# Kernel optimization log

Hardware: AMD Instinct MI355X
Metric: run time of the kernel (lower is better)

## Reference

```python
import jax, jax.numpy as jnp
import numpy as np

B, NT, DIM, HEADS = 8, 16, 768, 8
RES_H = RES_W = 32
PIX = RES_H * RES_W              # 1024
CHAN_NH = 16
NH = NW = 4                      # sqrt(chan_nheads)
WH, WW = RES_H // NH, RES_W // NW  # 8, 8
HEAD_DIM = DIM // HEADS          # 96
CHAN_HEAD_DIM = PIX // CHAN_NH   # 64


def _linear(x, w, b=None):
    y = x @ w.T
    return y if b is None else y + b


def _quat_kernel(r, i, j, k):
    # Hamilton-product block kernel: (4*out_c, 4*in_c, K)
    row_r = jnp.concatenate([r, -i, -j, -k], axis=1)
    row_i = jnp.concatenate([i, r, -k, j], axis=1)
    row_j = jnp.concatenate([j, k, r, -i], axis=1)
    row_k = jnp.concatenate([k, -j, i, r], axis=1)
    return jnp.concatenate([row_r, row_i, row_j, row_k], axis=0)


def _conv1d(x, w, b=None, pad=1):
    y = jax.lax.conv_general_dilated(x, w, (1,), [(pad, pad)],
                                     dimension_numbers=('NCH', 'OIH', 'NCH'))
    return y if b is None else y + b[None, :, None]


def _win(z, t):
    # 'b t (nh h nw w) -> b (nh nw) t (h w)'
    b = z.shape[0]
    z = z.reshape(b, t, NH, WH, NW, WW).transpose(0, 2, 4, 1, 3, 5)
    return z.reshape(b, NH * NW, t, WH * WW)


def setup_inputs():
    key = jax.random.key(0)
    ks = jax.random.split(key, 24)
    s = lambda i, shape: jax.random.normal(ks[i], shape, dtype=jnp.float32) * 0.02
    return dict(
        x=jax.random.normal(ks[0], (B, PIX, DIM), jnp.float32),
        task_prompts=jax.random.normal(ks[1], (B, NT, DIM), jnp.float32),
        qkv_w=s(2, (3 * DIM, DIM)),
        proj_w=s(3, (DIM, DIM)), proj_b=s(4, (DIM,)),
        tt_w=s(5, (PIX, DIM)), tt_b=s(6, (PIX,)),
        tt1_w=s(7, (DIM, PIX)), tt1_b=s(8, (DIM,)),
        qf_r=s(9, (2, 1, 3)), qf_i=s(10, (2, 1, 3)), qf_j=s(11, (2, 1, 3)),
        qf_k=s(12, (2, 1, 3)), qf_b=s(13, (8,)),
        dqf_r=s(14, (2, 1, 3)), dqf_i=s(15, (2, 1, 3)), dqf_j=s(16, (2, 1, 3)),
        dqf_k=s(17, (2, 1, 3)), dqf_b=s(18, (4,)),
        bn_g=jnp.ones((4,), jnp.float32), bn_b=jnp.zeros((4,), jnp.float32),
        qfto_w=s(19, (1, 4, 1)),
    )


def reference(x, task_prompts, qkv_w, proj_w, proj_b, tt_w, tt_b, tt1_w, tt1_b,
              qf_r, qf_i, qf_j, qf_k, qf_b, dqf_r, dqf_i, dqf_j, dqf_k, dqf_b,
              bn_g, bn_b, qfto_w):
    # ---- spatial attention over [prompts ; pixels] ----
    xc = jnp.concatenate([task_prompts, x], axis=1)           # (B, N, C), N = NT + PIX
    b, n, c = xc.shape
    qkv = _linear(xc, qkv_w).reshape(b, n, 3, HEADS, HEAD_DIM).transpose(2, 0, 3, 1, 4)
    q, k, v = qkv[0], qkv[1], qkv[2]
    raw_spa = jnp.einsum('bhqd,bhkd->bhqk', q, k)             # pre-scale logits (returned)
    spa_attn = jax.nn.softmax(raw_spa * HEAD_DIM ** -0.5, axis=-1)
    out = jnp.einsum('bhqk,bhkd->bhqd', spa_attn, v).transpose(0, 2, 1, 3).reshape(b, n, c)
    out = _linear(out, proj_w, proj_b)
    tp_out, x_out = out[:, :-PIX, :], out[:, -PIX:, :]        # sep_prompt(x, -pixel_no)

    # ---- windowed channel attention ----
    chan_x = x[:, -PIX:, :]                                   # (B, PIX, C)
    chan_prompts = _linear(task_prompts, tt_w, tt_b)          # (B, NT, PIX)
    qw = _win(chan_prompts, NT)                               # (B, 16, NT, 64)
    kw = _win(chan_x.transpose(0, 2, 1), DIM)                 # (B, 16, C, 64)
    raw_chan = jnp.einsum('bwtd,bwcd->bwtc', qw, kw)          # (B, 16, NT, C)
    chan_attn = jax.nn.softmax(raw_chan * CHAN_HEAD_DIM ** -0.5, axis=-1)
    # chan_x output of attn@v is computed in torch but unused downstream; XLA DCEs it.
    raw_chan_r = raw_chan.reshape(b, NH, NW, NT, DIM).transpose(0, 3, 4, 1, 2)   # b t c nh nw
    chan_attn_r = chan_attn.reshape(b, NH, NW, NT, DIM).transpose(0, 3, 4, 1, 2)

    # ---- quaternion fusion of prompt streams (vectorized over the torch per-sample loop) ----
    ch_prompts = _linear(chan_prompts, tt1_w, tt1_b)          # (B, NT, C)
    zero = jnp.zeros_like(tp_out)
    quater = jnp.stack([zero, task_prompts, tp_out, ch_prompts], axis=2)  # (B, NT, 4, C)
    w1 = _quat_kernel(qf_r, qf_i, qf_j, qf_k)                 # (8, 4, 3), OIH
    fe = _conv1d(quater.reshape(b * NT, 4, DIM), w1, qf_b)    # (B*NT, 8, C)
    w2 = _quat_kernel(dqf_r, dqf_i, dqf_j, dqf_k)             # (8, 4, 3) as (in, out, K)
    w2c = jnp.flip(w2, -1).transpose(1, 0, 2)                 # conv_transpose1d(s=1,p=1) == conv1d(flip, p=K-1-1)
    fe = _conv1d(fe, w2c, dqf_b).reshape(b, NT, 4, DIM)       # (B, NT, 4, C)
    # BatchNorm1d(4) in training mode, stats per loop iteration => per-sample over (NT, C)
    mean = fe.mean(axis=(1, 3), keepdims=True)
    var = fe.var(axis=(1, 3), keepdims=True)
    fe = (fe - mean) / jnp.sqrt(var + 1e-5) * bn_g[None, None, :, None] + bn_b[None, None, :, None]
    fe = jax.nn.gelu(fe, approximate=False)
    quater_out = jnp.einsum('bnkc,k->bnc', fe, qfto_w[0, :, 0])  # Conv1d(4,1,k=1,no bias)
    return (x_out, raw_spa, spa_attn, raw_chan_r, chan_attn_r, quater_out)
```

## Files before the change

kernel.cpp:

```cpp
#include <hip/hip_runtime.h>
#include <hip/hip_bf16.h>
#include <math.h>

typedef unsigned short u16;
typedef __attribute__((ext_vector_type(8))) short  bf16x8;
typedef __attribute__((ext_vector_type(4))) float  f32x4;
typedef __attribute__((ext_vector_type(8))) u16    u16x8;
typedef __attribute__((ext_vector_type(4))) u16    u16x4;

#define B_      8
#define NT_     16
#define DIM_    768
#define HEADS_  8
#define HD_     96
#define PIX_    1024
#define NTOK_   1040
#define NPAD_   1152

#define WSO_XCB     0ull
#define WSO_WQKV    12779520ull
#define WSO_WPROJ   16318464ull
#define WSO_QB      17498112ull
#define WSO_KB      31653888ull
#define WSO_VB      45809664ull
// ... 58 lines not shown
    if (bx < 3120) {
        size_t idx8 = ((size_t)bx * 256 + tid) * 8;
        int c = idx8 % DIM_;
        int n = (idx8 / DIM_) % NTOK_;
        int b = idx8 / ((size_t)DIM_ * NTOK_);
        s = (n < NT_) ? tp + ((size_t)b * NT_ + n) * DIM_ + c
                      : x + ((size_t)b * PIX_ + (n - NT_)) * DIM_ + c;
        d8 = xcb + idx8;
    } else {
        int i = (bx - 3120) * 256 + tid;
        const float* src;
        u16* dst;
        int li;
        if (i < 221184)      { src = qkv_w;  dst = wqkvb;  li = i; }
        else if (i < 294912) { src = proj_w; dst = wprojb; li = i - 221184; }
        else if (i < 307200) { src = tp;     dst = tpb;    li = i - 294912; }
        else if (i < 405504) { src = tt_w;   dst = ttwb;   li = i - 307200; }
        else if (i < 503808) { src = tt1_w;  dst = tt1wb;  li = i - 405504; }
        else return;
        s = src + (size_t)li * 8;
        d8 = dst + (size_t)li * 8;
    }
    float4 a = *(const float4*)s;
    float4 d = *(const float4*)(s + 4);
    u16x8 r;
    r[0] = f2b(a.x); r[1] = f2b(a.y); r[2] = f2b(a.z); r[3] = f2b(a.w);
    r[4] = f2b(d.x); r[5] = f2b(d.y); r[6] = f2b(d.z); r[7] = f2b(d.w);
    *(u16x8*)d8 = r;
}

template <int MODE>
__global__ __launch_bounds__(256) void gemm_bf16(
    const u16* __restrict__ A, const u16* __restrict__ Bw,
    int lda, int ldb, int K, size_t strA, size_t strB,
    const float* __restrict__ bias,
    float* __restrict__ o0, float* __restrict__ o1,
    u16* __restrict__ oq, u16* __restrict__ ok, u16* __restrict__ ov,
    int ldo) {
    __shared__ u16 As[128 * 32];
    __shared__ u16 Bs[128 * 32];
    __shared__ float redm[128][2];
    __shared__ float reds[128][2];
    const int tid = threadIdx.x;
    const int bm = blockIdx.x, bn = blockIdx.y, z = blockIdx.z;
    const u16* Ab = A + strA * z;
    const u16* Bb = Bw + strB * z;
    const int lane = tid & 63, wid = tid >> 6;
    const int ln = lane & 15, hi = lane >> 4;
    const int wr = wid >> 1, wc = wid & 1;
    const int lrow = lane >> 2;
    const int lcol = (lane & 3) * 8;
    f32x4 acc[4][4] = {};
    for (int kt = 0; kt < K; kt += 32) {
        __syncthreads();
#pragma unroll
        for (int t = 0; t < 2; ++t) {
            int rowbase = t * 64 + wid * 16;
            const u16* ga = Ab + (size_t)(bm * 128 + rowbase + lrow) * lda + kt + lcol;
            const u16* gb = Bb + (size_t)(bn * 128 + rowbase + lrow) * ldb + kt + lcol;
            gload_lds16(ga, &As[rowbase * 32]);
            gload_lds16(gb, &Bs[rowbase * 32]);
        }
        __syncthreads();
        bf16x8 af[4], bfr[4];
#pragma unroll
        for (int m = 0; m < 4; ++m)
            af[m] = *(const bf16x8*)&As[(wr * 64 + m * 16 + ln) * 32 + hi * 8];
#pragma unroll
        for (int n = 0; n < 4; ++n)
            bfr[n] = *(const bf16x8*)&Bs[(wc * 64 + n * 16 + ln) * 32 + hi * 8];
#pragma unroll
        for (int m = 0; m < 4; ++m)
#pragma unroll
            for (int n = 0; n < 4; ++n)
                acc[m][n] = __builtin_amdgcn_mfma_f32_16x16x32_bf16(af[m], bfr[n], acc[m][n], 0, 0, 0);
    }
#pragma unroll
    for (int m = 0; m < 4; ++m) {
#pragma unroll
        for (int n = 0; n < 4; ++n) {
#pragma unroll
            for (int j = 0; j < 4; ++j) {
                int gm = bm * 128 + wr * 64 + m * 16 + hi * 4 + j;
                int gn = bn * 128 + wc * 64 + n * 16 + ln;
                float v = acc[m][n][j];
                if (MODE == 0) {
                    int b = gm / NTOK_, nn = gm - b * NTOK_;
                    int s = gn / DIM_, rem = gn - s * DIM_;
                    int h = rem / HD_, d = rem - h * HD_;
                    u16 hv = f2b(v);
                    u16* dst = (s == 0) ? oq : (s == 1) ? ok : ov;
                    dst[(((size_t)b * HEADS_ + h) * NPAD_ + nn) * HD_ + d] = hv;
                } else if (MODE == 1) {
                    if (gm < NTOK_ && gn < NTOK_)
                        __builtin_nontemporal_store(v, &o0[((size_t)z * NTOK_ + gm) * NTOK_ + gn]);
                } else if (MODE == 2) {
                    v += bias[gn];
                    int b = gm / NTOK_, nn = gm - b * NTOK_;
                    if (nn < NT_) o1[((size_t)b * NT_ + nn) * DIM_ + gn] = v;
                    else          __builtin_nontemporal_store(v, &o0[((size_t)b * PIX_ + (nn - NT_)) * DIM_ + gn]);
                } else if (MODE == 3) {
                    oq[(size_t)gm * ldo + gn] = f2b(v + bias[gn]);
                } else {
                    o0[(size_t)gm * ldo + gn] = v + bias[gn];
                }
            }
        }
    }
    if (MODE == 1) {
#pragma unroll
        for (int m = 0; m < 4; ++m) {
#pragma unroll
            for (int j = 0; j < 4; ++j) {
                float v[4];
                float mx = -INFINITY;
#pragma unroll
                for (int n = 0; n < 4; ++n) {
                    int gn = bn * 128 + wc * 64 + n * 16 + ln;
                    v[n] = (gn < NTOK_) ? acc[m][n][j] * SCALE_SPA : -INFINITY;
                    mx = fmaxf(mx, v[n]);
                }
#pragma unroll
                for (int off = 1; off < 16; off <<= 1) mx = fmaxf(mx, __shfl_xor(mx, off));
                float s = 0.f;
                if (mx > -INFINITY) {
#pragma unroll
                    for (int n = 0; n < 4; ++n)
                        if (v[n] > -INFINITY) s += __expf(v[n] - mx);
                }
#pragma unroll
                for (int off = 1; off < 16; off <<= 1) s += __shfl_xor(s, off);
                if (ln == 0) {
                    int row = wr * 64 + m * 16 + hi * 4 + j;
                    redm[row][wc] = mx;
                    reds[row][wc] = s;
                }
            }
        }
        __syncthreads();
        if (tid < 128) {
            float m0 = redm[tid][0], m1 = redm[tid][1];
            float s0 = reds[tid][0], s1 = reds[tid][1];
            float M = fmaxf(m0, m1);
            float S = 0.f;
            if (m0 > -INFINITY) S += s0 * __expf(m0 - M);
            if (m1 > -INFINITY) S += s1 * __expf(m1 - M);
            float2* pp = (float2*)o1;
            pp[((size_t)z * 9 + bn) * NPAD_ + bm * 128 + tid] = make_float2(M, S);
        }
    }
}

__global__ __launch_bounds__(256) void transpose_v(const u16* __restrict__ vb,
                                                   u16* __restrict__ vtb) {
    __shared__ u16 t[32][34];
    int bi = blockIdx.x, bj = blockIdx.y, z = blockIdx.z;
    const u16* ib = vb + (size_t)z * NPAD_ * HD_;
    u16* ob = vtb + (size_t)z * HD_ * NPAD_;
    int tid = threadIdx.x;
    int r = tid >> 3, c = (tid & 7) * 4;
    *(u16x4*)&t[r][c] = *(const u16x4*)(ib + (size_t)(bi * 32 + r) * HD_ + bj * 32 + c);
    __syncthreads();
    u16x4 o;
    o[0] = t[c + 0][r]; o[1] = t[c + 1][r]; o[2] = t[c + 2][r]; o[3] = t[c + 3][r];
    *(u16x4*)(ob + (size_t)(bj * 32 + r) * NPAD_ + bi * 32 + c) = o;
}

__global__ __launch_bounds__(256) void attn_pv4(const float* __restrict__ raw,
                                                const float2* __restrict__ part,
                                                const u16* __restrict__ vtb,
                                                float* __restrict__ attn,
                                                u16* __restrict__ acat) {
    __shared__ u16 Ps[64][136];
    __shared__ float sm[64], si[64];
    const int tid = threadIdx.x;
    const int bi = blockIdx.x, z = blockIdx.y;
    const int lane = tid & 63, wid = tid >> 6;
    const int ln = lane & 15, hi = lane >> 4;
    const int wr = wid >> 1, wc = wid & 1;
    const int r0 = tid >> 3, c8 = tid & 7;
    const u16* vbz = vtb + (size_t)z * HD_ * NPAD_;
    const float* rawz = raw + (size_t)z * NTOK_ * NTOK_;
    float* attnz = attn + (size_t)z * NTOK_ * NTOK_;
    int rows[2];
    bool vr[2];
#pragma unroll
    for (int p = 0; p < 2; ++p) {
        rows[p] = bi * 64 + p * 32 + r0;
        vr[p] = rows[p] < NTOK_;
    }
    f32x4 rcur[4][2], rnxt[4][2];
#pragma unroll
    for (int s = 0; s < 4; ++s) {
        int col = s * 32 + c8 * 4;
#pragma unroll
        for (int p = 0; p < 2; ++p) {
            f32x4 zv = {0.f, 0.f, 0.f, 0.f};
            if (vr[p] && col < NTOK_)
                zv = __builtin_nontemporal_load((const f32x4*)(rawz + (size_t)rows[p] * NTOK_ + col));
            rcur[s][p] = zv;
        }
    }
    if (tid < 64) {
        int grow = bi * 64 + tid;
        float M = -INFINITY;
        float mj[9], sj[9];
#pragma unroll
        for (int jt = 0; jt < 9; ++jt) {
            float2 p = part[((size_t)z * 9 + jt) * NPAD_ + grow];
            mj[jt] = p.x; sj[jt] = p.y;
            M = fmaxf(M, p.x);
        }
        float S = 0.f;
#pragma unroll
        for (int jt = 0; jt < 9; ++jt)
            if (mj[jt] > -INFINITY) S += sj[jt] * __expf(mj[jt] - M);
        sm[tid] = M;
        si[tid] = 1.f / S;
    }
    __syncthreads();
    float mr[2], ir[2];
#pragma unroll
    for (int p = 0; p < 2; ++p) {
        mr[p] = sm[p * 32 + r0];
        ir[p] = si[p * 32 + r0];
    }
    f32x4 oacc[2][3] = {};
    for (int ci = 0; ci < 9; ++ci) {
        const int c0 = ci * 128;
#pragma unroll
        for (int s = 0; s < 4; ++s) {
            int cl = s * 32 + c8 * 4;
            int col = c0 + cl;
#pragma unroll
            for (int p = 0; p < 2; ++p) {
                int rr = p * 32 + r0;
                u16x4 pb = {0, 0, 0, 0};
                if (vr[p] && col < NTOK_) {
                    f32x4 v = rcur[s][p];
                    f32x4 pr;
                    pr[0] = __expf(v[0] * SCALE_SPA - mr[p]) * ir[p];
                    pr[1] = __expf(v[1] * SCALE_SPA - mr[p]) * ir[p];
                    pr[2] = __expf(v[2] * SCALE_SPA - mr[p]) * ir[p];
                    pr[3] = __expf(v[3] * SCALE_SPA - mr[p]) * ir[p];
                    __builtin_nontemporal_store(pr, (f32x4*)(attnz + (size_t)rows[p] * NTOK_ + col));
                    pb[0] = f2b_fast(pr[0]); pb[1] = f2b_fast(pr[1]);
                    pb[2] = f2b_fast(pr[2]); pb[3] = f2b_fast(pr[3]);
                }
                *(u16x4*)&Ps[rr][cl] = pb;
            }
        }
        if (ci < 8) {
#pragma unroll
            for (int s = 0; s < 4; ++s) {
                int col = c0 + 128 + s * 32 + c8 * 4;
#pragma unroll
                for (int p = 0; p < 2; ++p) {
                    f32x4 zv = {0.f, 0.f, 0.f, 0.f};
                    if (vr[p] && col < NTOK_)
                        zv = __builtin_nontemporal_load((const f32x4*)(rawz + (size_t)rows[p] * NTOK_ + col));
                    rnxt[s][p] = zv;
                }
            }
        }
        __syncthreads();
#pragma unroll
        for (int ktl = 0; ktl < 4; ++ktl) {
            bf16x8 af[2];
#pragma unroll
            for (int m = 0; m < 2; ++m)
                af[m] = *(const bf16x8*)&Ps[wr * 32 + m * 16 + ln][ktl * 32 + hi * 8];
#pragma unroll
            for (int n = 0; n < 3; ++n) {
                bf16x8 bv = *(const bf16x8*)(vbz + (size_t)(wc * 48 + n * 16 + ln) * NPAD_
                                             + c0 + ktl * 32 + hi * 8);
#pragma unroll
                for (int m = 0; m < 2; ++m)
                    oacc[m][n] = __builtin_amdgcn_mfma_f32_16x16x32_bf16(af[m], bv, oacc[m][n], 0, 0, 0);
            }
        }
        __syncthreads();
#pragma unroll
        for (int s = 0; s < 4; ++s)
#pragma unroll
            for (int p = 0; p < 2; ++p)
                rcur[s][p] = rnxt[s][p];
    }
    const int b = z >> 3, h = z & 7;
#pragma unroll
    for (int m = 0; m < 2; ++m)
#pragma unroll
        for (int n = 0; n < 3; ++n)
#pragma unroll
            for (int j = 0; j < 4; ++j) {
                int gi = bi * 64 + wr * 32 + m * 16 + hi * 4 + j;
                if (gi < NTOK_) {
                    int gd = wc * 48 + n * 16 + ln;
                    acat[((size_t)b * NTOK_ + gi) * DIM_ + h * HD_ + gd] = f2b(oacc[m][n][j]);
                }
            }
}

__global__ __launch_bounds__(256) void chan_scores(const u16* __restrict__ chanpb,
                                                   const float* __restrict__ x,
                                                   float* __restrict__ rawchan_ws,
                                                   float* __restrict__ out_raw) {
    int blk = blockIdx.x;
    int b = blk / 16, w = blk % 16;
    int cy = blockIdx.y;
    int nh = w / 4, nw = w % 4;
    __shared__ float qp[16][65];
    __shared__ float xs[64][17];
    int tid = threadIdx.x;
    for (int l = tid; l < 16 * 64; l += 256) {
        int t = l / 64, d = l % 64;
        int wh = d / 8, ww = d % 8;
        int pix = (nh * 8 + wh) * 32 + nw * 8 + ww;
        qp[t][d] = b2f(chanpb[((size_t)b * NT_ + t) * PIX_ + pix]);
    }
    __syncthreads();
    int t = tid % 16, cl = tid / 16;
    for (int cc = cy * 8; cc < cy * 8 + 8; ++cc) {
        for (int l = tid; l < 64 * 16; l += 256) {
            int d = l / 16, c2 = l % 16;
            int wh = d / 8, ww = d % 8;
            int pix = (nh * 8 + wh) * 32 + nw * 8 + ww;
            xs[d][c2] = x[((size_t)b * PIX_ + pix) * DIM_ + cc * 16 + c2];
        }
        __syncthreads();
        float acc = 0.f;
#pragma unroll
        for (int d = 0; d < 64; ++d) acc += qp[t][d] * xs[d][cl];
        int c = cc * 16 + cl;
        rawchan_ws[(((size_t)b * 16 + w) * NT_ + t) * DIM_ + c] = acc;
        out_raw[(((size_t)b * NT_ + t) * DIM_ + c) * 16 + w] = acc;
        __syncthreads();
    }
}

__global__ __launch_bounds__(256) void chan_softmax(const float* __restrict__ rawchan_ws,
                                                    float* __restrict__ out_attn) {
    int row = blockIdx.x;
    int b = row / 256;
    int w = (row / 16) % 16;
    int t = row % 16;
    const float* rp = rawchan_ws + (size_t)row * DIM_;
    int tid = threadIdx.x;
    float vals[3];
    float m = -INFINITY;
#pragma unroll
    for (int i = 0; i < 3; ++i) {
        vals[i] = rp[tid + i * 256] * 0.125f;
        m = fmaxf(m, vals[i]);
    }
    __shared__ float redm[4], reds[4];
    for (int off = 32; off; off >>= 1) m = fmaxf(m, __shfl_xor(m, off));
    if ((tid & 63) == 0) redm[tid >> 6] = m;
    __syncthreads();
    m = fmaxf(fmaxf(redm[0], redm[1]), fmaxf(redm[2], redm[3]));
    float s = 0.f;
#pragma unroll
    for (int i = 0; i < 3; ++i) { vals[i] = __expf(vals[i] - m); s += vals[i]; }
    for (int off = 32; off; off >>= 1) s += __shfl_xor(s, off);
    if ((tid & 63) == 0) reds[tid >> 6] = s;
    __syncthreads();
    s = reds[0] + reds[1] + reds[2] + reds[3];
    float inv = 1.f / s;
#pragma unroll
    for (int i = 0; i < 3; ++i) {
        int c = tid + i * 256;
        out_attn[(((size_t)b * NT_ + t) * DIM_ + c) * 16 + w] = vals[i] * inv;
    }
}

__global__ __launch_bounds__(256) void quat_conv(const float* __restrict__ tp,
                                                 const float* __restrict__ tpo,
                                                 const float* __restrict__ chp,
                                                 const float* __restrict__ qf_r, const float* __restrict__ qf_i,
                                                 const float* __restrict__ qf_j, const float* __restrict__ qf_k,
                                                 const float* __restrict__ qf_b,
                                                 const float* __restrict__ dqf_r, const float* __restrict__ dqf_i,
                                                 const float* __restrict__ dqf_j, const float* __restrict__ dqf_k,
                                                 const float* __restrict__ dqf_b,
                                                 float* __restrict__ fe2_out,
                                                 float* __restrict__ partials) {
    int blk = blockIdx.x;
    int b = blk / NT_, t = blk % NT_;
    __shared__ float w1[8][4][3];
    __shared__ float w2[8][4][3];
    __shared__ float w2c[4][8][3];
    __shared__ float qs[4][770];
    __shared__ float fs[8][770];
    __shared__ float wsum[4][4], wsq[4][4];
    int tid = threadIdx.x;
    if (tid < 96) {
        int o = tid / 12, rest = tid % 12, ic = rest / 3, tap = rest % 3;
        int g = o / 2, oo = o % 2;
        const int   cidx[4][4] = {{0, 1, 2, 3}, {1, 0, 3, 2}, {2, 3, 0, 1}, {3, 2, 1, 0}};
        const float csgn[4][4] = {{1, -1, -1, -1}, {1, 1, -1, 1}, {1, 1, 1, -1}, {1, -1, 1, 1}};
        const float* s1[4] = {qf_r, qf_i, qf_j, qf_k};
        const float* s2[4] = {dqf_r, dqf_i, dqf_j, dqf_k};
        w1[o][ic][tap] = csgn[g][ic] * s1[cidx[g][ic]][oo * 3 + tap];
        w2[o][ic][tap] = csgn[g][ic] * s2[cidx[g][ic]][oo * 3 + tap];
    }
    for (int l = tid; l < DIM_; l += 256) {
        size_t base = ((size_t)b * NT_ + t) * DIM_ + l;
        qs[0][1 + l] = 0.f;
        qs[1][1 + l] = tp[base];
        qs[2][1 + l] = tpo[base];
        qs[3][1 + l] = chp[base];
    }
    if (tid < 4) { qs[tid][0] = 0.f; qs[tid][769] = 0.f; }
    if (tid < 8) { fs[tid][0] = 0.f; fs[tid][769] = 0.f; }
    __syncthreads();
    if (tid < 96) {
        int o2 = tid / 24, rest = tid % 24, i2 = rest / 3, tap = rest % 3;
        w2c[o2][i2][tap] = w2[i2][o2][2 - tap];
    }
    for (int l = tid; l < DIM_; l += 256) {
#pragma unroll
        for (int o = 0; o < 8; ++o) {
            float a = qf_b[o];
#pragma unroll
            for (int ic = 0; ic < 4; ++ic)
#pragma unroll
                for (int tap = 0; tap < 3; ++tap) a += w1[o][ic][tap] * qs[ic][l + tap];
            fs[o][1 + l] = a;
        }
    }
    __syncthreads();
    float lsum[4] = {}, lsq[4] = {};
    for (int l = tid; l < DIM_; l += 256) {
#pragma unroll
        for (int o2 = 0; o2 < 4; ++o2) {
            float a = dqf_b[o2];
#pragma unroll
            for (int i2 = 0; i2 < 8; ++i2)
#pragma unroll
                for (int tap = 0; tap < 3; ++tap) a += w2c[o2][i2][tap] * fs[i2][l + tap];
            fe2_out[((size_t)blk * 4 + o2) * DIM_ + l] = a;
            lsum[o2] += a;
            lsq[o2] += a * a;
        }
    }
    int wid = tid >> 6;
#pragma unroll
    for (int o2 = 0; o2 < 4; ++o2) {
        float s = lsum[o2], q = lsq[o2];
        for (int off = 32; off; off >>= 1) { s += __shfl_xor(s, off); q += __shfl_xor(q, off); }
        if ((tid & 63) == 0) { wsum[wid][o2] = s; wsq[wid][o2] = q; }
    }
    __syncthreads();
    if (tid < 4) {
        float s = wsum[0][tid] + wsum[1][tid] + wsum[2][tid] + wsum[3][tid];
        float q = wsq[0][tid] + wsq[1][tid] + wsq[2][tid] + wsq[3][tid];
        partials[(size_t)blk * 8 + tid * 2 + 0] = s;
        partials[(size_t)blk * 8 + tid * 2 + 1] = q;
    }
}

__global__ __launch_bounds__(256) void bn_gelu_out(const float* __restrict__ fe2,
                                                   const float* __restrict__ partials,
                                                   const float* __restrict__ bn_g,
                                                   const float* __restrict__ bn_b,
                                                   const float* __restrict__ qfto,
                                                   float* __restrict__ out5) {
    int blk = blockIdx.x;
    int b = blk / NT_;
    int tid = threadIdx.x;
    float mean[4], rstd[4], gam[4], bet[4], qw[4];
#pragma unroll
    for (int kk = 0; kk < 4; ++kk) {
        float s = 0.f, q = 0.f;
        for (int t2 = 0; t2 < 16; ++t2) {
            const float* p = partials + ((size_t)(b * NT_ + t2) * 8 + kk * 2);
            s += p[0];
            q += p[1];
        }
        float mu = s * (1.f / 12288.f);
        float var = q * (1.f / 12288.f) - mu * mu;
        mean[kk] = mu;
        rstd[kk] = rsqrtf(var + 1e-5f);
        gam[kk] = bn_g[kk];
        bet[kk] = bn_b[kk];
        qw[kk] = qfto[kk];
    }
    for (int l = tid; l < DIM_; l += 256) {
        float acc = 0.f;
#pragma unroll
        for (int kk = 0; kk < 4; ++kk) {
// ... 26 lines not shown
    const float* dqf_r  = (const float*)d_in[14];
    const float* dqf_i  = (const float*)d_in[15];
    const float* dqf_j  = (const float*)d_in[16];
    const float* dqf_k  = (const float*)d_in[17];
    const float* dqf_b  = (const float*)d_in[18];
    const float* bn_g   = (const float*)d_in[19];
    const float* bn_b   = (const float*)d_in[20];
    const float* qfto   = (const float*)d_in[21];
    float* out = (float*)d_out;
    char* wsb = (char*)d_ws;

    u16* xcb    = (u16*)(wsb + WSO_XCB);
    u16* wqkvb  = (u16*)(wsb + WSO_WQKV);
    u16* wprojb = (u16*)(wsb + WSO_WPROJ);
    u16* qb     = (u16*)(wsb + WSO_QB);
    u16* kb     = (u16*)(wsb + WSO_KB);
    u16* vb     = (u16*)(wsb + WSO_VB);
    u16* vtb    = (u16*)(wsb + WSO_VTB);
    u16* acatb  = (u16*)(wsb + WSO_ACATB);
    u16* tpb    = (u16*)(wsb + WSO_TPB);
    u16* ttwb   = (u16*)(wsb + WSO_TTWB);
    u16* tt1wb  = (u16*)(wsb + WSO_TT1WB);
    u16* chanpb = (u16*)(wsb + WSO_CHANPB);
    float* partb = (float*)(wsb + WSO_PART);
    float* f32r = (float*)(wsb + WSO_F32);
    float* tpout   = f32r + FO_TPOUT;
    float* rawchan = f32r + FO_RAWCHAN;
    float* chpf    = f32r + FO_CHP;
    float* fe2     = f32r + FO_FE2;
    float* stats   = f32r + FO_STATS;

    cast_fused<<<5088, 256, 0, stream>>>(tp, x, qkv_w, proj_w, tt_w, tt1_w,
                                         xcb, wqkvb, wprojb, tpb, ttwb, tt1wb);

    gemm_bf16<0><<<dim3(65, 18, 1), 256, 0, stream>>>(xcb, wqkvb, 768, 768, 768, 0, 0,
                                                      nullptr, nullptr, nullptr, qb, kb, vb, 0);
    transpose_v<<<dim3(36, 3, 64), 256, 0, stream>>>(vb, vtb);
    gemm_bf16<1><<<dim3(9, 9, 64), 256, 0, stream>>>(qb, kb, 96, 96, 96,
                                                     (size_t)NPAD_ * HD_, (size_t)NPAD_ * HD_,
                                                     nullptr, out + OUT_RAW, partb,
                                                     nullptr, nullptr, nullptr, 0);
    attn_pv4<<<dim3(17, 64), 256, 0, stream>>>(out + OUT_RAW, (const float2*)partb,
                                               vtb, out + OUT_ATTN, acatb);
    gemm_bf16<2><<<dim3(65, 6, 1), 256, 0, stream>>>(acatb, wprojb, 768, 768, 768, 0, 0,
                                                     proj_b, out + OUT_XOUT, tpout,
                                                     nullptr, nullptr, nullptr, 0);
    gemm_bf16<3><<<dim3(1, 8, 1), 256, 0, stream>>>(tpb, ttwb, 768, 768, 768, 0, 0,
                                                    tt_b, nullptr, nullptr, chanpb, nullptr, nullptr, 1024);
    chan_scores<<<dim3(128, 6), 256, 0, stream>>>(chanpb, x, rawchan, out + OUT_RAWCH);
    chan_softmax<<<2048, 256, 0, stream>>>(rawchan, out + OUT_ATTNCH);
    gemm_bf16<4><<<dim3(1, 6, 1), 256, 0, stream>>>(chanpb, tt1wb, 1024, 1024, 1024, 0, 0,
                                                    tt1_b, chpf, nullptr, nullptr, nullptr, nullptr, 768);
    quat_conv<<<128, 256, 0, stream>>>(tp, tpout, chpf,
                                       qf_r, qf_i, qf_j, qf_k, qf_b,
                                       dqf_r, dqf_i, dqf_j, dqf_k, dqf_b,
                                       fe2, stats);
    bn_gelu_out<<<128, 256, 0, stream>>>(fe2, stats, bn_g, bn_b, qfto, out + OUT_QOUT);
}
```

Before: 487.9 us.

## Merge independent kernels into combined launches via block-index dispatch

Independent stages are packed into shared launches that branch on block index. The scores GEMM shares a launch with the V transpose, PV attention with channel scores, and the quaternion conv with channel softmax. The channel-prompt GEMM is also moved earlier so its consumer can share a launch with PV. This cuts launch count and lets small, underfilled kernels fill spare CUs alongside larger ones, at the cost of more shared-memory and register pressure per block.

```diff
diff --git a/kernel.cpp b/kernel.cpp
--- a/kernel.cpp
+++ b/kernel.cpp
@@ -114,19 +114,15 @@
 template <int MODE>
 __global__ __launch_bounds__(256) void gemm_bf16(
     const u16* __restrict__ A, const u16* __restrict__ Bw,
-    int lda, int ldb, int K, size_t strA, size_t strB,
+    int lda, int ldb, int K,
     const float* __restrict__ bias,
     float* __restrict__ o0, float* __restrict__ o1,
     u16* __restrict__ oq, u16* __restrict__ ok, u16* __restrict__ ov,
     int ldo) {
     __shared__ u16 As[128 * 32];
     __shared__ u16 Bs[128 * 32];
-    __shared__ float redm[128][2];
-    __shared__ float reds[128][2];
     const int tid = threadIdx.x;
-    const int bm = blockIdx.x, bn = blockIdx.y, z = blockIdx.z;
-    const u16* Ab = A + strA * z;
-    const u16* Bb = Bw + strB * z;
+    const int bm = blockIdx.x, bn = blockIdx.y;
     const int lane = tid & 63, wid = tid >> 6;
     const int ln = lane & 15, hi = lane >> 4;
     const int wr = wid >> 1, wc = wid & 1;
@@ -138,8 +134,8 @@
 #pragma unroll
         for (int t = 0; t < 2; ++t) {
             int rowbase = t * 64 + wid * 16;
-            const u16* ga = Ab + (size_t)(bm * 128 + rowbase + lrow) * lda + kt + lcol;
-            const u16* gb = Bb + (size_t)(bn * 128 + rowbase + lrow) * ldb + kt + lcol;
+            const u16* ga = A + (size_t)(bm * 128 + rowbase + lrow) * lda + kt + lcol;
+            const u16* gb = Bw + (size_t)(bn * 128 + rowbase + lrow) * ldb + kt + lcol;
             gload_lds16(ga, &As[rowbase * 32]);
             gload_lds16(gb, &Bs[rowbase * 32]);
         }
@@ -173,9 +169,6 @@
                     u16 hv = f2b(v);
                     u16* dst = (s == 0) ? oq : (s == 1) ? ok : ov;
                     dst[(((size_t)b * HEADS_ + h) * NPAD_ + nn) * HD_ + d] = hv;
-                } else if (MODE == 1) {
-                    if (gm < NTOK_ && gn < NTOK_)
-                        __builtin_nontemporal_store(v, &o0[((size_t)z * NTOK_ + gm) * NTOK_ + gn]);
                 } else if (MODE == 2) {
                     v += bias[gn];
                     int b = gm / NTOK_, nn = gm - b * NTOK_;
@@ -189,7 +182,65 @@
             }
         }
     }
-    if (MODE == 1) {
+}
+
+__global__ __launch_bounds__(256) void k_scores_vt(const u16* __restrict__ qb,
+                                                   const u16* __restrict__ kb,
+                                                   float* __restrict__ raw,
+                                                   float2* __restrict__ part,
+                                                   const u16* __restrict__ vb,
+                                                   u16* __restrict__ vtb) {
+    __shared__ u16 As[128 * 32];
+    __shared__ u16 Bs[128 * 32];
+    __shared__ float redm[128][2];
+    __shared__ float reds[128][2];
+    const int bx = blockIdx.x, tid = threadIdx.x;
+    if (bx < 5184) {
+        const int bm = bx % 9, bn = (bx / 9) % 9, z = bx / 81;
+        const u16* Ab = qb + (size_t)z * NPAD_ * HD_;
+        const u16* Bb = kb + (size_t)z * NPAD_ * HD_;
+        const int lane = tid & 63, wid = tid >> 6;
+        const int ln = lane & 15, hi = lane >> 4;
+        const int wr = wid >> 1, wc = wid & 1;
+        const int lrow = lane >> 2;
+        const int lcol = (lane & 3) * 8;
+        f32x4 acc[4][4] = {};
+        for (int kt = 0; kt < 96; kt += 32) {
+            __syncthreads();
+#pragma unroll
+            for (int t = 0; t < 2; ++t) {
+                int rowbase = t * 64 + wid * 16;
+                const u16* ga = Ab + (size_t)(bm * 128 + rowbase + lrow) * HD_ + kt + lcol;
+                const u16* gb = Bb + (size_t)(bn * 128 + rowbase + lrow) * HD_ + kt + lcol;
+                gload_lds16(ga, &As[rowbase * 32]);
+                gload_lds16(gb, &Bs[rowbase * 32]);
+            }
+            __syncthreads();
+            bf16x8 af[4], bfr[4];
+#pragma unroll
+            for (int m = 0; m < 4; ++m)
+                af[m] = *(const bf16x8*)&As[(wr * 64 + m * 16 + ln) * 32 + hi * 8];
+#pragma unroll
+            for (int n = 0; n < 4; ++n)
+                bfr[n] = *(const bf16x8*)&Bs[(wc * 64 + n * 16 + ln) * 32 + hi * 8];
+#pragma unroll
+            for (int m = 0; m < 4; ++m)
+#pragma unroll
+                for (int n = 0; n < 4; ++n)
+                    acc[m][n] = __builtin_amdgcn_mfma_f32_16x16x32_bf16(af[m], bfr[n], acc[m][n], 0, 0, 0);
+        }
+#pragma unroll
+        for (int m = 0; m < 4; ++m)
+#pragma unroll
+            for (int n = 0; n < 4; ++n)
+#pragma unroll
+                for (int j = 0; j < 4; ++j) {
+                    int gm = bm * 128 + wr * 64 + m * 16 + hi * 4 + j;
+                    int gn = bn * 128 + wc * 64 + n * 16 + ln;
+                    if (gm < NTOK_ && gn < NTOK_)
+                        __builtin_nontemporal_store(acc[m][n][j],
+                            &raw[((size_t)z * NTOK_ + gm) * NTOK_ + gn]);
+                }
 #pragma unroll
         for (int m = 0; m < 4; ++m) {
 #pragma unroll
@@ -227,317 +278,316 @@
             float S = 0.f;
             if (m0 > -INFINITY) S += s0 * __expf(m0 - M);
             if (m1 > -INFINITY) S += s1 * __expf(m1 - M);
-            float2* pp = (float2*)o1;
-            pp[((size_t)z * 9 + bn) * NPAD_ + bm * 128 + tid] = make_float2(M, S);
-        }
+            part[((size_t)z * 9 + bn) * NPAD_ + bm * 128 + tid] = make_float2(M, S);
+        }
+    } else {
+        u16 (*t)[34] = (u16(*)[34])As;
+        int idx = bx - 5184;
+        int bi = idx % 36, bj = (idx / 36) % 3, z = idx / 108;
+        const u16* ib = vb + (size_t)z * NPAD_ * HD_;
+        u16* ob = vtb + (size_t)z * HD_ * NPAD_;
+        int r = tid >> 3, c = (tid & 7) * 4;
+        *(u16x4*)&t[r][c] = *(const u16x4*)(ib + (size_t)(bi * 32 + r) * HD_ + bj * 32 + c);
+        __syncthreads();
+        u16x4 o;
+        o[0] = t[c + 0][r]; o[1] = t[c + 1][r]; o[2] = t[c + 2][r]; o[3] = t[c + 3][r];
+        *(u16x4*)(ob + (size_t)(bj * 32 + r) * NPAD_ + bi * 32 + c) = o;
     }
 }
 
-__global__ __launch_bounds__(256) void transpose_v(const u16* __restrict__ vb,
-                                                   u16* __restrict__ vtb) {
-    __shared__ u16 t[32][34];
-    int bi = blockIdx.x, bj = blockIdx.y, z = blockIdx.z;
-    const u16* ib = vb + (size_t)z * NPAD_ * HD_;
-    u16* ob = vtb + (size_t)z * HD_ * NPAD_;
-    int tid = threadIdx.x;
-    int r = tid >> 3, c = (tid & 7) * 4;
-    *(u16x4*)&t[r][c] = *(const u16x4*)(ib + (size_t)(bi * 32 + r) * HD_ + bj * 32 + c);
-    __syncthreads();
-    u16x4 o;
-    o[0] = t[c + 0][r]; o[1] = t[c + 1][r]; o[2] = t[c + 2][r]; o[3] = t[c + 3][r];
-    *(u16x4*)(ob + (size_t)(bj * 32 + r) * NPAD_ + bi * 32 + c) = o;
-}
-
-__global__ __launch_bounds__(256) void attn_pv4(const float* __restrict__ raw,
-                                                const float2* __restrict__ part,
-                                                const u16* __restrict__ vtb,
-                                                float* __restrict__ attn,
-                                                u16* __restrict__ acat) {
-    __shared__ u16 Ps[64][136];
-    __shared__ float sm[64], si[64];
-    const int tid = threadIdx.x;
-    const int bi = blockIdx.x, z = blockIdx.y;
-    const int lane = tid & 63, wid = tid >> 6;
-    const int ln = lane & 15, hi = lane >> 4;
-    const int wr = wid >> 1, wc = wid & 1;
-    const int r0 = tid >> 3, c8 = tid & 7;
-    const u16* vbz = vtb + (size_t)z * HD_ * NPAD_;
-    const float* rawz = raw + (size_t)z * NTOK_ * NTOK_;
-    float* attnz = attn + (size_t)z * NTOK_ * NTOK_;
-    int rows[2];
-    bool vr[2];
-#pragma unroll
-    for (int p = 0; p < 2; ++p) {
-        rows[p] = bi * 64 + p * 32 + r0;
-        vr[p] = rows[p] < NTOK_;
-    }
-    f32x4 rcur[4][2], rnxt[4][2];
-#pragma unroll
-    for (int s = 0; s < 4; ++s) {
-        int col = s * 32 + c8 * 4;
-#pragma unroll
-        for (int p = 0; p < 2; ++p) {
-            f32x4 zv = {0.f, 0.f, 0.f, 0.f};
-            if (vr[p] && col < NTOK_)
-                zv = __builtin_nontemporal_load((const f32x4*)(rawz + (size_t)rows[p] * NTOK_ + col));
-            rcur[s][p] = zv;
-        }
-    }
-    if (tid < 64) {
-        int grow = bi * 64 + tid;
-        float M = -INFINITY;
-        float mj[9], sj[9];
-#pragma unroll
-        for (int jt = 0; jt < 9; ++jt) {
-            float2 p = part[((size_t)z * 9 + jt) * NPAD_ + grow];
-            mj[jt] = p.x; sj[jt] = p.y;
-            M = fmaxf(M, p.x);
-        }
-        float S = 0.f;
-#pragma unroll
-        for (int jt = 0; jt < 9; ++jt)
-            if (mj[jt] > -INFINITY) S += sj[jt] * __expf(mj[jt] - M);
-        sm[tid] = M;
-        si[tid] = 1.f / S;
-    }
-    __syncthreads();
-    float mr[2], ir[2];
-#pragma unroll
-    for (int p = 0; p < 2; ++p) {
-        mr[p] = sm[p * 32 + r0];
-        ir[p] = si[p * 32 + r0];
-    }
-    f32x4 oacc[2][3] = {};
-    for (int ci = 0; ci < 9; ++ci) {
-        const int c0 = ci * 128;
-#pragma unroll
-        for (int s = 0; s < 4; ++s) {
-            int cl = s * 32 + c8 * 4;
-            int col = c0 + cl;
-#pragma unroll
-            for (int p = 0; p < 2; ++p) {
-                int rr = p * 32 + r0;
-                u16x4 pb = {0, 0, 0, 0};
-                if (vr[p] && col < NTOK_) {
-                    f32x4 v = rcur[s][p];
-                    f32x4 pr;
-                    pr[0] = __expf(v[0] * SCALE_SPA - mr[p]) * ir[p];
-                    pr[1] = __expf(v[1] * SCALE_SPA - mr[p]) * ir[p];
-                    pr[2] = __expf(v[2] * SCALE_SPA - mr[p]) * ir[p];
-                    pr[3] = __expf(v[3] * SCALE_SPA - mr[p]) * ir[p];
-                    __builtin_nontemporal_store(pr, (f32x4*)(attnz + (size_t)rows[p] * NTOK_ + col));
-                    pb[0] = f2b_fast(pr[0]); pb[1] = f2b_fast(pr[1]);
-                    pb[2] = f2b_fast(pr[2]); pb[3] = f2b_fast(pr[3]);
-                }
-                *(u16x4*)&Ps[rr][cl] = pb;
-            }
-        }
-        if (ci < 8) {
-#pragma unroll
-            for (int s = 0; s < 4; ++s) {
-                int col = c0 + 128 + s * 32 + c8 * 4;
-#pragma unroll
-                for (int p = 0; p < 2; ++p) {
-                    f32x4 zv = {0.f, 0.f, 0.f, 0.f};
-                    if (vr[p] && col < NTOK_)
-                        zv = __builtin_nontemporal_load((const f32x4*)(rawz + (size_t)rows[p] * NTOK_ + col));
-                    rnxt[s][p] = zv;
-                }
-            }
-        }
-        __syncthreads();
-#pragma unroll
-        for (int ktl = 0; ktl < 4; ++ktl) {
-            bf16x8 af[2];
-#pragma unroll
-            for (int m = 0; m < 2; ++m)
-                af[m] = *(const bf16x8*)&Ps[wr * 32 + m * 16 + ln][ktl * 32 + hi * 8];
-#pragma unroll
-            for (int n = 0; n < 3; ++n) {
-                bf16x8 bv = *(const bf16x8*)(vbz + (size_t)(wc * 48 + n * 16 + ln) * NPAD_
-                                             + c0 + ktl * 32 + hi * 8);
-#pragma unroll
-                for (int m = 0; m < 2; ++m)
-                    oacc[m][n] = __builtin_amdgcn_mfma_f32_16x16x32_bf16(af[m], bv, oacc[m][n], 0, 0, 0);
-            }
-        }
-        __syncthreads();
-#pragma unroll
-        for (int s = 0; s < 4; ++s)
-#pragma unroll
-            for (int p = 0; p < 2; ++p)
-                rcur[s][p] = rnxt[s][p];
-    }
-    const int b = z >> 3, h = z & 7;
-#pragma unroll
-    for (int m = 0; m < 2; ++m)
-#pragma unroll
-        for (int n = 0; n < 3; ++n)
-#pragma unroll
-            for (int j = 0; j < 4; ++j) {
-                int gi = bi * 64 + wr * 32 + m * 16 + hi * 4 + j;
-                if (gi < NTOK_) {
-                    int gd = wc * 48 + n * 16 + ln;
-                    acat[((size_t)b * NTOK_ + gi) * DIM_ + h * HD_ + gd] = f2b(oacc[m][n][j]);
-                }
-            }
-}
-
-__global__ __launch_bounds__(256) void chan_scores(const u16* __restrict__ chanpb,
+__global__ __launch_bounds__(256) void k_pv_chansc(const float* __restrict__ raw,
+                                                   const float2* __restrict__ part,
+                                                   const u16* __restrict__ vtb,
+                                                   float* __restrict__ attn,
+                                                   u16* __restrict__ acat,
+                                                   const u16* __restrict__ chanpb,
                                                    const float* __restrict__ x,
                                                    float* __restrict__ rawchan_ws,
                                                    float* __restrict__ out_raw) {
-    int blk = blockIdx.x;
-    int b = blk / 16, w = blk % 16;
-    int cy = blockIdx.y;
-    int nh = w / 4, nw = w % 4;
-    __shared__ float qp[16][65];
-    __shared__ float xs[64][17];
-    int tid = threadIdx.x;
-    for (int l = tid; l < 16 * 64; l += 256) {
-        int t = l / 64, d = l % 64;
-        int wh = d / 8, ww = d % 8;
-        int pix = (nh * 8 + wh) * 32 + nw * 8 + ww;
-        qp[t][d] = b2f(chanpb[((size_t)b * NT_ + t) * PIX_ + pix]);
-    }
-    __syncthreads();
-    int t = tid % 16, cl = tid / 16;
-    for (int cc = cy * 8; cc < cy * 8 + 8; ++cc) {
-        for (int l = tid; l < 64 * 16; l += 256) {
-            int d = l / 16, c2 = l % 16;
+    __shared__ __align__(16) char smem[17920 + 512];
+    const int bx = blockIdx.x, tid = threadIdx.x;
+    if (bx < 1088) {
+        u16 (*Ps)[136] = (u16(*)[136])smem;
+        float* sm = (float*)(smem + 17408);
+        float* si = sm + 64;
+        const int bi = bx % 17, z = bx / 17;
+        const int lane = tid & 63, wid = tid >> 6;
+        const int ln = lane & 15, hi = lane >> 4;
+        const int wr = wid >> 1, wc = wid & 1;
+        const int r0 = tid >> 3, c8 = tid & 7;
+        const u16* vbz = vtb + (size_t)z * HD_ * NPAD_;
+        const float* rawz = raw + (size_t)z * NTOK_ * NTOK_;
+        float* attnz = attn + (size_t)z * NTOK_ * NTOK_;
+        int rows[2];
+        bool vr[2];
+#pragma unroll
+        for (int p = 0; p < 2; ++p) {
+            rows[p] = bi * 64 + p * 32 + r0;
+            vr[p] = rows[p] < NTOK_;
+        }
+        f32x4 rcur[4][2], rnxt[4][2];
+#pragma unroll
+        for (int s = 0; s < 4; ++s) {
+            int col = s * 32 + c8 * 4;
+#pragma unroll
+            for (int p = 0; p < 2; ++p) {
+                f32x4 zv = {0.f, 0.f, 0.f, 0.f};
+                if (vr[p] && col < NTOK_)
+                    zv = __builtin_nontemporal_load((const f32x4*)(rawz + (size_t)rows[p] * NTOK_ + col));
+                rcur[s][p] = zv;
+            }
+        }
+        if (tid < 64) {
+            int grow = bi * 64 + tid;
+            float M = -INFINITY;
+            float mj[9], sj[9];
+#pragma unroll
+            for (int jt = 0; jt < 9; ++jt) {
+                float2 p = part[((size_t)z * 9 + jt) * NPAD_ + grow];
+                mj[jt] = p.x; sj[jt] = p.y;
+                M = fmaxf(M, p.x);
+            }
+            float S = 0.f;
+#pragma unroll
+            for (int jt = 0; jt < 9; ++jt)
+                if (mj[jt] > -INFINITY) S += sj[jt] * __expf(mj[jt] - M);
+            sm[tid] = M;
+            si[tid] = 1.f / S;
+        }
+        __syncthreads();
+        float mr[2], ir[2];
+#pragma unroll
+        for (int p = 0; p < 2; ++p) {
+            mr[p] = sm[p * 32 + r0];
+            ir[p] = si[p * 32 + r0];
+        }
+        f32x4 oacc[2][3] = {};
+        for (int ci = 0; ci < 9; ++ci) {
+            const int c0 = ci * 128;
+#pragma unroll
+            for (int s = 0; s < 4; ++s) {
+                int cl = s * 32 + c8 * 4;
+                int col = c0 + cl;
+#pragma unroll
+                for (int p = 0; p < 2; ++p) {
+                    int rr = p * 32 + r0;
+                    u16x4 pb = {0, 0, 0, 0};
+                    if (vr[p] && col < NTOK_) {
+                        f32x4 v = rcur[s][p];
+                        f32x4 pr;
+                        pr[0] = __expf(v[0] * SCALE_SPA - mr[p]) * ir[p];
+                        pr[1] = __expf(v[1] * SCALE_SPA - mr[p]) * ir[p];
+                        pr[2] = __expf(v[2] * SCALE_SPA - mr[p]) * ir[p];
+                        pr[3] = __expf(v[3] * SCALE_SPA - mr[p]) * ir[p];
+                        __builtin_nontemporal_store(pr, (f32x4*)(attnz + (size_t)rows[p] * NTOK_ + col));
+                        pb[0] = f2b_fast(pr[0]); pb[1] = f2b_fast(pr[1]);
+                        pb[2] = f2b_fast(pr[2]); pb[3] = f2b_fast(pr[3]);
+                    }
+                    *(u16x4*)&Ps[rr][cl] = pb;
+                }
+            }
+            if (ci < 8) {
+#pragma unroll
+                for (int s = 0; s < 4; ++s) {
+                    int col = c0 + 128 + s * 32 + c8 * 4;
+#pragma unroll
+                    for (int p = 0; p < 2; ++p) {
+                        f32x4 zv = {0.f, 0.f, 0.f, 0.f};
+                        if (vr[p] && col < NTOK_)
+                            zv = __builtin_nontemporal_load((const f32x4*)(rawz + (size_t)rows[p] * NTOK_ + col));
+                        rnxt[s][p] = zv;
+                    }
+                }
+            }
+            __syncthreads();
+#pragma unroll
+            for (int ktl = 0; ktl < 4; ++ktl) {
+                bf16x8 af[2];
+#pragma unroll
+                for (int m = 0; m < 2; ++m)
+                    af[m] = *(const bf16x8*)&Ps[wr * 32 + m * 16 + ln][ktl * 32 + hi * 8];
+#pragma unroll
+                for (int n = 0; n < 3; ++n) {
+                    bf16x8 bv = *(const bf16x8*)(vbz + (size_t)(wc * 48 + n * 16 + ln) * NPAD_
+                                                 + c0 + ktl * 32 + hi * 8);
+#pragma unroll
+                    for (int m = 0; m < 2; ++m)
+                        oacc[m][n] = __builtin_amdgcn_mfma_f32_16x16x32_bf16(af[m], bv, oacc[m][n], 0, 0, 0);
+                }
+            }
+            __syncthreads();
+#pragma unroll
+            for (int s = 0; s < 4; ++s)
+#pragma unroll
+                for (int p = 0; p < 2; ++p)
+                    rcur[s][p] = rnxt[s][p];
+        }
+        const int b = z >> 3, h = z & 7;
+#pragma unroll
+        for (int m = 0; m < 2; ++m)
+#pragma unroll
+            for (int n = 0; n < 3; ++n)
+#pragma unroll
+                for (int j = 0; j < 4; ++j) {
+                    int gi = bi * 64 + wr * 32 + m * 16 + hi * 4 + j;
+                    if (gi < NTOK_) {
+                        int gd = wc * 48 + n * 16 + ln;
+                        acat[((size_t)b * NTOK_ + gi) * DIM_ + h * HD_ + gd] = f2b(oacc[m][n][j]);
+                    }
+                }
+    } else {
+        float (*qp)[65] = (float(*)[65])smem;
+        float (*xs)[17] = (float(*)[17])(smem + 4160);
+        int idx = bx - 1088;
+        int blk = idx % 128, cy = idx / 128;
+        int b = blk / 16, w = blk % 16;
+        int nh = w / 4, nw = w % 4;
+        for (int l = tid; l < 16 * 64; l += 256) {
+            int t = l / 64, d = l % 64;
             int wh = d / 8, ww = d % 8;
             int pix = (nh * 8 + wh) * 32 + nw * 8 + ww;
-            xs[d][c2] = x[((size_t)b * PIX_ + pix) * DIM_ + cc * 16 + c2];
-        }
-        __syncthreads();
-        float acc = 0.f;
-#pragma unroll
-        for (int d = 0; d < 64; ++d) acc += qp[t][d] * xs[d][cl];
-        int c = cc * 16 + cl;
-        rawchan_ws[(((size_t)b * 16 + w) * NT_ + t) * DIM_ + c] = acc;
-        out_raw[(((size_t)b * NT_ + t) * DIM_ + c) * 16 + w] = acc;
-        __syncthreads();
+            qp[t][d] = b2f(chanpb[((size_t)b * NT_ + t) * PIX_ + pix]);
+        }
+        __syncthreads();
+        int t = tid % 16, cl = tid / 16;
+        for (int cc = cy * 8; cc < cy * 8 + 8; ++cc) {
+            for (int l = tid; l < 64 * 16; l += 256) {
+                int d = l / 16, c2 = l % 16;
+                int wh = d / 8, ww = d % 8;
+                int pix = (nh * 8 + wh) * 32 + nw * 8 + ww;
+                xs[d][c2] = x[((size_t)b * PIX_ + pix) * DIM_ + cc * 16 + c2];
+            }
+            __syncthreads();
+            float acc = 0.f;
+#pragma unroll
+            for (int d = 0; d < 64; ++d) acc += qp[t][d] * xs[d][cl];
+            int c = cc * 16 + cl;
+            rawchan_ws[(((size_t)b * 16 + w) * NT_ + t) * DIM_ + c] = acc;
+            out_raw[(((size_t)b * NT_ + t) * DIM_ + c) * 16 + w] = acc;
+            __syncthreads();
+        }
     }
 }
 
-__global__ __launch_bounds__(256) void chan_softmax(const float* __restrict__ rawchan_ws,
-                                                    float* __restrict__ out_attn) {
-    int row = blockIdx.x;
-    int b = row / 256;
-    int w = (row / 16) % 16;
-    int t = row % 16;
-    const float* rp = rawchan_ws + (size_t)row * DIM_;
-    int tid = threadIdx.x;
-    float vals[3];
-    float m = -INFINITY;
-#pragma unroll
-    for (int i = 0; i < 3; ++i) {
-        vals[i] = rp[tid + i * 256] * 0.125f;
-        m = fmaxf(m, vals[i]);
-    }
-    __shared__ float redm[4], reds[4];
-    for (int off = 32; off; off >>= 1) m = fmaxf(m, __shfl_xor(m, off));
-    if ((tid & 63) == 0) redm[tid >> 6] = m;
-    __syncthreads();
-    m = fmaxf(fmaxf(redm[0], redm[1]), fmaxf(redm[2], redm[3]));
-    float s = 0.f;
-#pragma unroll
-    for (int i = 0; i < 3; ++i) { vals[i] = __expf(vals[i] - m); s += vals[i]; }
-    for (int off = 32; off; off >>= 1) s += __shfl_xor(s, off);
-    if ((tid & 63) == 0) reds[tid >> 6] = s;
-    __syncthreads();
-    s = reds[0] + reds[1] + reds[2] + reds[3];
-    float inv = 1.f / s;
-#pragma unroll
-    for (int i = 0; i < 3; ++i) {
-        int c = tid + i * 256;
-        out_attn[(((size_t)b * NT_ + t) * DIM_ + c) * 16 + w] = vals[i] * inv;
-    }
-}
-
-__global__ __launch_bounds__(256) void quat_conv(const float* __restrict__ tp,
-                                                 const float* __restrict__ tpo,
-                                                 const float* __restrict__ chp,
-                                                 const float* __restrict__ qf_r, const float* __restrict__ qf_i,
-                                                 const float* __restrict__ qf_j, const float* __restrict__ qf_k,
-                                                 const float* __restrict__ qf_b,
-                                                 const float* __restrict__ dqf_r, const float* __restrict__ dqf_i,
-                                                 const float* __restrict__ dqf_j, const float* __restrict__ dqf_k,
-                                                 const float* __restrict__ dqf_b,
-                                                 float* __restrict__ fe2_out,
-                                                 float* __restrict__ partials) {
-    int blk = blockIdx.x;
-    int b = blk / NT_, t = blk % NT_;
+__global__ __launch_bounds__(256) void k_quat_chansm(const float* __restrict__ tp,
+                                                     const float* __restrict__ tpo,
+                                                     const float* __restrict__ chp,
+                                                     const float* __restrict__ qf_r, const float* __restrict__ qf_i,
+                                                     const float* __restrict__ qf_j, const float* __restrict__ qf_k,
+                                                     const float* __restrict__ qf_b,
+                                                     const float* __restrict__ dqf_r, const float* __restrict__ dqf_i,
+                                                     const float* __restrict__ dqf_j, const float* __restrict__ dqf_k,
+                                                     const float* __restrict__ dqf_b,
+                                                     float* __restrict__ fe2_out,
+                                                     float* __restrict__ partials,
+                                                     const float* __restrict__ rawchan_ws,
+                                                     float* __restrict__ out_attn) {
     __shared__ float w1[8][4][3];
     __shared__ float w2[8][4][3];
     __shared__ float w2c[4][8][3];
     __shared__ float qs[4][770];
     __shared__ float fs[8][770];
     __shared__ float wsum[4][4], wsq[4][4];
+    __shared__ float srm[4], srs[4];
+    const int bx = blockIdx.x;
     int tid = threadIdx.x;
-    if (tid < 96) {
-        int o = tid / 12, rest = tid % 12, ic = rest / 3, tap = rest % 3;
-        int g = o / 2, oo = o % 2;
-        const int   cidx[4][4] = {{0, 1, 2, 3}, {1, 0, 3, 2}, {2, 3, 0, 1}, {3, 2, 1, 0}};
-        const float csgn[4][4] = {{1, -1, -1, -1}, {1, 1, -1, 1}, {1, 1, 1, -1}, {1, -1, 1, 1}};
-        const float* s1[4] = {qf_r, qf_i, qf_j, qf_k};
-        const float* s2[4] = {dqf_r, dqf_i, dqf_j, dqf_k};
-        w1[o][ic][tap] = csgn[g][ic] * s1[cidx[g][ic]][oo * 3 + tap];
-        w2[o][ic][tap] = csgn[g][ic] * s2[cidx[g][ic]][oo * 3 + tap];
-    }
-    for (int l = tid; l < DIM_; l += 256) {
-        size_t base = ((size_t)b * NT_ + t) * DIM_ + l;
-        qs[0][1 + l] = 0.f;
-        qs[1][1 + l] = tp[base];
-        qs[2][1 + l] = tpo[base];
-        qs[3][1 + l] = chp[base];
-    }
-    if (tid < 4) { qs[tid][0] = 0.f; qs[tid][769] = 0.f; }
-    if (tid < 8) { fs[tid][0] = 0.f; fs[tid][769] = 0.f; }
-    __syncthreads();
-    if (tid < 96) {
-        int o2 = tid / 24, rest = tid % 24, i2 = rest / 3, tap = rest % 3;
-        w2c[o2][i2][tap] = w2[i2][o2][2 - tap];
-    }
-    for (int l = tid; l < DIM_; l += 256) {
-#pragma unroll
-        for (int o = 0; o < 8; ++o) {
-            float a = qf_b[o];
-#pragma unroll
-            for (int ic = 0; ic < 4; ++ic)
-#pragma unroll
-                for (int tap = 0; tap < 3; ++tap) a += w1[o][ic][tap] * qs[ic][l + tap];
-            fs[o][1 + l] = a;
-        }
-    }
-    __syncthreads();
-    float lsum[4] = {}, lsq[4] = {};
-    for (int l = tid; l < DIM_; l += 256) {
+    if (bx < 128) {
+        int blk = bx;
+        int b = blk / NT_, t = blk % NT_;
+        if (tid < 96) {
+            int o = tid / 12, rest = tid % 12, ic = rest / 3, tap = rest % 3;
+            int g = o / 2, oo = o % 2;
+            const int   cidx[4][4] = {{0, 1, 2, 3}, {1, 0, 3, 2}, {2, 3, 0, 1}, {3, 2, 1, 0}};
+            const float csgn[4][4] = {{1, -1, -1, -1}, {1, 1, -1, 1}, {1, 1, 1, -1}, {1, -1, 1, 1}};
+            const float* s1[4] = {qf_r, qf_i, qf_j, qf_k};
+            const float* s2[4] = {dqf_r, dqf_i, dqf_j, dqf_k};
+            w1[o][ic][tap] = csgn[g][ic] * s1[cidx[g][ic]][oo * 3 + tap];
+            w2[o][ic][tap] = csgn[g][ic] * s2[cidx[g][ic]][oo * 3 + tap];
+        }
+        for (int l = tid; l < DIM_; l += 256) {
+            size_t base = ((size_t)b * NT_ + t) * DIM_ + l;
+            qs[0][1 + l] = 0.f;
+            qs[1][1 + l] = tp[base];
+            qs[2][1 + l] = tpo[base];
+            qs[3][1 + l] = chp[base];
+        }
+        if (tid < 4) { qs[tid][0] = 0.f; qs[tid][769] = 0.f; }
+        if (tid < 8) { fs[tid][0] = 0.f; fs[tid][769] = 0.f; }
+        __syncthreads();
+        if (tid < 96) {
+            int o2 = tid / 24, rest = tid % 24, i2 = rest / 3, tap = rest % 3;
+            w2c[o2][i2][tap] = w2[i2][o2][2 - tap];
+        }
+        for (int l = tid; l < DIM_; l += 256) {
+#pragma unroll
+            for (int o = 0; o < 8; ++o) {
+                float a = qf_b[o];
+#pragma unroll
+                for (int ic = 0; ic < 4; ++ic)
+#pragma unroll
+                    for (int tap = 0; tap < 3; ++tap) a += w1[o][ic][tap] * qs[ic][l + tap];
+                fs[o][1 + l] = a;
+            }
+        }
+        __syncthreads();
+        float lsum[4] = {}, lsq[4] = {};
+        for (int l = tid; l < DIM_; l += 256) {
+#pragma unroll
+            for (int o2 = 0; o2 < 4; ++o2) {
+                float a = dqf_b[o2];
+#pragma unroll
+                for (int i2 = 0; i2 < 8; ++i2)
+#pragma unroll
+                    for (int tap = 0; tap < 3; ++tap) a += w2c[o2][i2][tap] * fs[i2][l + tap];
+                fe2_out[((size_t)blk * 4 + o2) * DIM_ + l] = a;
+                lsum[o2] += a;
+                lsq[o2] += a * a;
+            }
+        }
+        int wid = tid >> 6;
 #pragma unroll
         for (int o2 = 0; o2 < 4; ++o2) {
-            float a = dqf_b[o2];
-#pragma unroll
-            for (int i2 = 0; i2 < 8; ++i2)
-#pragma unroll
-                for (int tap = 0; tap < 3; ++tap) a += w2c[o2][i2][tap] * fs[i2][l + tap];
-            fe2_out[((size_t)blk * 4 + o2) * DIM_ + l] = a;
-            lsum[o2] += a;
-            lsq[o2] += a * a;
-        }
-    }
-    int wid = tid >> 6;
-#pragma unroll
-    for (int o2 = 0; o2 < 4; ++o2) {
-        float s = lsum[o2], q = lsq[o2];
-        for (int off = 32; off; off >>= 1) { s += __shfl_xor(s, off); q += __shfl_xor(q, off); }
-        if ((tid & 63) == 0) { wsum[wid][o2] = s; wsq[wid][o2] = q; }
-    }
-    __syncthreads();
-    if (tid < 4) {
-        float s = wsum[0][tid] + wsum[1][tid] + wsum[2][tid] + wsum[3][tid];
-        float q = wsq[0][tid] + wsq[1][tid] + wsq[2][tid] + wsq[3][tid];
-        partials[(size_t)blk * 8 + tid * 2 + 0] = s;
-        partials[(size_t)blk * 8 + tid * 2 + 1] = q;
+            float s = lsum[o2], q = lsq[o2];
+            for (int off = 32; off; off >>= 1) { s += __shfl_xor(s, off); q += __shfl_xor(q, off); }
+            if ((tid & 63) == 0) { wsum[wid][o2] = s; wsq[wid][o2] = q; }
+        }
+        __syncthreads();
+        if (tid < 4) {
+            float s = wsum[0][tid] + wsum[1][tid] + wsum[2][tid] + wsum[3][tid];
+            float q = wsq[0][tid] + wsq[1][tid] + wsq[2][tid] + wsq[3][tid];
+            partials[(size_t)blk * 8 + tid * 2 + 0] = s;
+            partials[(size_t)blk * 8 + tid * 2 + 1] = q;
+        }
+    } else {
+        int row = bx - 128;
+        int b = row / 256;
+        int w = (row / 16) % 16;
+        int t = row % 16;
+        const float* rp = rawchan_ws + (size_t)row * DIM_;
+        float vals[3];
+        float m = -INFINITY;
+#pragma unroll
+        for (int i = 0; i < 3; ++i) {
+            vals[i] = rp[tid + i * 256] * 0.125f;
+            m = fmaxf(m, vals[i]);
+        }
+        for (int off = 32; off; off >>= 1) m = fmaxf(m, __shfl_xor(m, off));
+        if ((tid & 63) == 0) srm[tid >> 6] = m;
+        __syncthreads();
+        m = fmaxf(fmaxf(srm[0], srm[1]), fmaxf(srm[2], srm[3]));
+        float s = 0.f;
+#pragma unroll
+        for (int i = 0; i < 3; ++i) { vals[i] = __expf(vals[i] - m); s += vals[i]; }
+        for (int off = 32; off; off >>= 1) s += __shfl_xor(s, off);
+        if ((tid & 63) == 0) srs[tid >> 6] = s;
+        __syncthreads();
+        s = srs[0] + srs[1] + srs[2] + srs[3];
+        float inv = 1.f / s;
+#pragma unroll
+        for (int i = 0; i < 3; ++i) {
+            int c = tid + i * 256;
+            out_attn[(((size_t)b * NT_ + t) * DIM_ + c) * 16 + w] = vals[i] * inv;
+        }
     }
 }
 
@@ -630,28 +680,22 @@
 
     cast_fused<<<5088, 256, 0, stream>>>(tp, x, qkv_w, proj_w, tt_w, tt1_w,
                                          xcb, wqkvb, wprojb, tpb, ttwb, tt1wb);
-
-    gemm_bf16<0><<<dim3(65, 18, 1), 256, 0, stream>>>(xcb, wqkvb, 768, 768, 768, 0, 0,
-                                                      nullptr, nullptr, nullptr, qb, kb, vb, 0);
-    transpose_v<<<dim3(36, 3, 64), 256, 0, stream>>>(vb, vtb);
-    gemm_bf16<1><<<dim3(9, 9, 64), 256, 0, stream>>>(qb, kb, 96, 96, 96,
-                                                     (size_t)NPAD_ * HD_, (size_t)NPAD_ * HD_,
-                                                     nullptr, out + OUT_RAW, partb,
-                                                     nullptr, nullptr, nullptr, 0);
-    attn_pv4<<<dim3(17, 64), 256, 0, stream>>>(out + OUT_RAW, (const float2*)partb,
-                                               vtb, out + OUT_ATTN, acatb);
-    gemm_bf16<2><<<dim3(65, 6, 1), 256, 0, stream>>>(acatb, wprojb, 768, 768, 768, 0, 0,
-                                                     proj_b, out + OUT_XOUT, tpout,
-                                                     nullptr, nullptr, nullptr, 0);
-    gemm_bf16<3><<<dim3(1, 8, 1), 256, 0, stream>>>(tpb, ttwb, 768, 768, 768, 0, 0,
-                                                    tt_b, nullptr, nullptr, chanpb, nullptr, nullptr, 1024);
-    chan_scores<<<dim3(128, 6), 256, 0, stream>>>(chanpb, x, rawchan, out + OUT_RAWCH);
-    chan_softmax<<<2048, 256, 0, stream>>>(rawchan, out + OUT_ATTNCH);
-    gemm_bf16<4><<<dim3(1, 6, 1), 256, 0, stream>>>(chanpb, tt1wb, 1024, 1024, 1024, 0, 0,
-                                                    tt1_b, chpf, nullptr, nullptr, nullptr, nullptr, 768);
-    quat_conv<<<128, 256, 0, stream>>>(tp, tpout, chpf,
-                                       qf_r, qf_i, qf_j, qf_k, qf_b,
-                                       dqf_r, dqf_i, dqf_j, dqf_k, dqf_b,
-                                       fe2, stats);
+    gemm_bf16<0><<<dim3(65, 18), 256, 0, stream>>>(xcb, wqkvb, 768, 768, 768,
+                                                   nullptr, nullptr, nullptr, qb, kb, vb, 0);
+    gemm_bf16<3><<<dim3(1, 8), 256, 0, stream>>>(tpb, ttwb, 768, 768, 768,
+                                                 tt_b, nullptr, nullptr, chanpb, nullptr, nullptr, 1024);
+    k_scores_vt<<<12096, 256, 0, stream>>>(qb, kb, out + OUT_RAW, (float2*)partb, vb, vtb);
+    k_pv_chansc<<<1856, 256, 0, stream>>>(out + OUT_RAW, (const float2*)partb, vtb,
+                                          out + OUT_ATTN, acatb,
+                                          chanpb, x, rawchan, out + OUT_RAWCH);
+    gemm_bf16<2><<<dim3(65, 6), 256, 0, stream>>>(acatb, wprojb, 768, 768, 768,
+                                                  proj_b, out + OUT_XOUT, tpout,
+                                                  nullptr, nullptr, nullptr, 0);
+    gemm_bf16<4><<<dim3(1, 6), 256, 0, stream>>>(chanpb, tt1wb, 1024, 1024, 1024,
+                                                 tt1_b, chpf, nullptr, nullptr, nullptr, nullptr, 768);
+    k_quat_chansm<<<2176, 256, 0, stream>>>(tp, tpout, chpf,
+                                            qf_r, qf_i, qf_j, qf_k, qf_b,
+                                            dqf_r, dqf_i, dqf_j, dqf_k, dqf_b,
+                                            fe2, stats, rawchan, out + OUT_ATTNCH);
     bn_gelu_out<<<128, 256, 0, stream>>>(fe2, stats, bn_g, bn_b, qfto, out + OUT_QOUT);
 }
```

Result: slower. 500.2 us (+2.5%).
